# Kernel tuning notes

Hardware: AMD Instinct MI355X
Metric: run time of the kernel (lower is better)

The kernel has to match this reference:

```python
import jax, jax.numpy as jnp
import numpy as np

VOCAB, EMB, LAT, MAXLEN, BATCH = 2048, 256, 64, 32, 64
SIZE_LAT = 3.0  # size_lat_dim: initial upper bound of every latent dimension


def setup_inputs() -> dict:
    key = jax.random.key(0)
    k0, k1, k2, k3 = jax.random.split(key, 4)
    tokens = jax.random.randint(k0, (BATCH, MAXLEN), 1, VOCAB, dtype=jnp.int32)  # avoid PAD=0
    emb = jax.random.normal(k1, (VOCAB, EMB), jnp.float32) * 0.02
    Wx = jax.random.normal(k2, (EMB, 4 * VOCAB), jnp.float32) * (1.0 / np.sqrt(EMB))
    Wh = jax.random.normal(k3, (VOCAB, 4 * VOCAB), jnp.float32) * (1.0 / np.sqrt(VOCAB))
    b = jnp.zeros((4 * VOCAB,), jnp.float32)
    return {"tokens": tokens, "emb": emb, "Wx": Wx, "Wh": Wh, "b": b}


def _lstm_step(x, h, c, Wx, Wh, b):
    # Keras LSTM gate order: i, f, g(candidate), o
    z = x @ Wx + h @ Wh + b
    i, f, g, o = jnp.split(z, 4, axis=-1)
    c = jax.nn.sigmoid(f) * c + jax.nn.sigmoid(i) * jnp.tanh(g)
    h = jax.nn.sigmoid(o) * jnp.tanh(c)
    return h, c


def reference(tokens, emb, Wx, Wh, b):
    B = tokens.shape[0]
    low0 = jnp.zeros((B, LAT), jnp.float32)
    upp0 = jnp.full((B, LAT), SIZE_LAT, jnp.float32)
    h0 = jnp.zeros((B, VOCAB), jnp.float32)  # empty (all-PAD) prefix -> zero LSTM output -> uniform softmax
    c0 = jnp.zeros((B, VOCAB), jnp.float32)
    dims = jnp.arange(LAT)

    def step(carry, tok):
        low, upp, h, c, d = carry
        # LM distribution over next token given prefix consumed so far
        probs = jax.nn.softmax(h, axis=-1)                      # [B, V]
        cum = jnp.cumsum(probs, axis=-1)
        c_upp = jnp.take_along_axis(cum, tok[:, None], axis=-1)[:, 0]
        c_low = c_upp - jnp.take_along_axis(probs, tok[:, None], axis=-1)[:, 0]
        # arithmetic-coding bound update on current latent dimension d only
        mask = dims == d                                         # [LAT]
        rng = jnp.sum(jnp.where(mask, upp - low, 0.0), axis=-1)  # [B] range at dim d
        base = jnp.sum(jnp.where(mask, low, 0.0), axis=-1)       # [B] low at dim d
        low = jnp.where(mask[None, :], (base + rng * c_low)[:, None], low)
        upp = jnp.where(mask[None, :], (base + rng * c_upp)[:, None], upp)
        z = 0.5 * (low + upp)                                    # mean of stacked bounds
        # advance embedded LM by one token (equivalent to re-running it on the prefix)
        h, c = _lstm_step(emb[tok], h, c, Wx, Wh, b)
        d = (d + 1) % LAT
        return (low, upp, h, c, d), z

    _, zs = jax.lax.scan(step, (low0, upp0, h0, c0, jnp.int32(0)), tokens.T)
    return jnp.transpose(zs, (1, 0, 2))  # [B, MAXLEN, LAT]
```

## Files before the change

### kernel.cpp

```cpp
#include <hip/hip_runtime.h>
#include <hip/hip_bf16.h>

#define VOCAB 2048
#define EMBD  256
#define KTOT  2304
#define LATD  64
#define TLEN  32
#define BATCH 64
#define NBLK  256
#define NCG   128
#define AROW  2304
#define ASLOT (BATCH * AROW)

typedef __attribute__((ext_vector_type(4))) float f32x4;

__global__ void k_init(unsigned char* __restrict__ a8, unsigned* __restrict__ bar) {
  int i = blockIdx.x * 256 + threadIdx.x;
  if (i < 32768) {
    int row = i >> 9;
    *(unsigned*)(a8 + (size_t)row * AROW + ((i & 511) << 2)) = 0u;
  }
  if (i < 384) bar[i] = 0;
}

__global__ void k_conv(const float* __restrict__ src,
                       unsigned char* __restrict__ dst, int koff) {
  __shared__ unsigned char tile[64][80];
  int k0 = (blockIdx.x >> 7) * 64;
  int n0 = (blockIdx.x & 127) * 64;
  int tid = threadIdx.x;
  {
    int kl = tid >> 2;
    int nq = (tid & 3) << 4;
    const float* s = src + (size_t)(k0 + kl) * 8192 + n0 + nq;
#pragma unroll
    for (int i = 0; i < 4; ++i) {
      float4 v = *reinterpret_cast<const float4*>(s + i * 4);
      unsigned pa = (unsigned)__builtin_amdgcn_cvt_pk_fp8_f32(v.x * 32.f, v.y * 32.f, 0, false);
      unsigned pb = (unsigned)__builtin_amdgcn_cvt_pk_fp8_f32(v.z * 32.f, v.w * 32.f, 0, false);
      tile[nq + i * 4 + 0][kl] = (unsigned char)(pa & 0xFF);
      tile[nq + i * 4 + 1][kl] = (unsigned char)((pa >> 8) & 0xFF);
      tile[nq + i * 4 + 2][kl] = (unsigned char)(pb & 0xFF);
      tile[nq + i * 4 + 3][kl] = (unsigned char)((pb >> 8) & 0xFF);
    }
  }
  __syncthreads();
  {
    int nl = tid >> 2;
    int kq = (tid & 3) << 4;
    *(uint4*)(dst + (size_t)(n0 + nl) * AROW + koff + k0 + kq) =
        *(const uint4*)&tile[nl][kq];
  }
}

__global__ void k_gather(const int* __restrict__ tokens,
                         const float* __restrict__ emb,
                         unsigned char* __restrict__ a8) {
  int tid = threadIdx.x;
  int row = blockIdx.x * 4 + (tid >> 6);
  int lane = tid & 63;
  int t = row >> 6, b = row & 63;
  int tok = tokens[b * TLEN + t];
  float4 v = *reinterpret_cast<const float4*>(emb + (size_t)tok * EMBD + lane * 4);
  unsigned pa = (unsigned)__builtin_amdgcn_cvt_pk_fp8_f32(v.x * 256.f, v.y * 256.f, 0, false);
  unsigned pb = (unsigned)__builtin_amdgcn_cvt_pk_fp8_f32(v.z * 256.f, v.w * 256.f, 0, false);
  *(unsigned*)(a8 + (size_t)t * ASLOT + (size_t)b * AROW + 2048 + lane * 4) =
      (pa & 0xFFFFu) | (pb << 16);
}

__device__ __forceinline__ void store_agent_u32(unsigned* p, unsigned v) {
  __hip_atomic_store(p, v, __ATOMIC_RELAXED, __HIP_MEMORY_SCOPE_AGENT);
}
__device__ __forceinline__ unsigned load_agent_u32(const unsigned* p) {
  return __hip_atomic_load(p, __ATOMIC_RELAXED, __HIP_MEMORY_SCOPE_AGENT);
}
__device__ __forceinline__ unsigned long long load_agent_u64(const void* p) {
  return __hip_atomic_load((const unsigned long long*)p, __ATOMIC_RELAXED,
                           __HIP_MEMORY_SCOPE_AGENT);
}
__device__ __forceinline__ void store_agent_f32(float* p, float v) {
  __hip_atomic_store(p, v, __ATOMIC_RELAXED, __HIP_MEMORY_SCOPE_AGENT);
}
__device__ __forceinline__ float2 load_agent_f32x2(const float* p) {
  unsigned long long u = load_agent_u64(p);
  float2 f;
  __builtin_memcpy(&f, &u, 8);
  return f;
}

__device__ __forceinline__ void grid_barrier(unsigned* arrv, unsigned* rel,
                                             int t, int j, int tid, int lane) {
  __syncthreads();
  const unsigned want = (unsigned)(t + 1);
  if (j == 0) {
    if (tid < 64) {
      if (lane == 0) store_agent_u32(arrv, want);
      for (;;) {
        unsigned long long a = load_agent_u64(arrv + 2 * lane);
        unsigned long long b = load_agent_u64(arrv + 128 + 2 * lane);
        bool ok = ((unsigned)a >= want) && ((unsigned)(a >> 32) >= want) &&
                  ((unsigned)b >= want) && ((unsigned)(b >> 32) >= want);
        if (__all(ok)) break;
      }
      if (lane < 8) store_agent_u32(rel + (lane << 4), want);
    }
  } else {
    if (tid == 0) {
      store_agent_u32(arrv + j, want);
      while (load_agent_u32(rel + ((j & 7) << 4)) < want)
        __builtin_amdgcn_s_sleep(1);
    }
  }
  __syncthreads();
}

__global__ __launch_bounds__(512, 1) void k_persist(
    const int* __restrict__ tokens,
    const unsigned char* __restrict__ B8,
    unsigned char* __restrict__ a8,
    const float* __restrict__ bias,
    float* __restrict__ stats,
    float* __restrict__ out,
    unsigned* __restrict__ arrv,
    unsigned* __restrict__ rel) {
  const int tid = threadIdx.x;
  const int lane = tid & 63;
  const int wid = tid >> 6;
  const int j = blockIdx.x;
  const int cg = (j & 7) | ((j >> 4) << 3);
  const int rg = (j >> 3) & 1;
  const int r0 = rg << 5;

  __shared__ float racc[8][2][4][4][64];
  __shared__ float spart[TLEN][3];
  __shared__ float sval[TLEN];

  const int rr = lane & 15;
  const int kg = lane >> 4;

  long Bf[9][4];
  {
    const unsigned char* b8B[4];
#pragma unroll
    for (int gt = 0; gt < 4; ++gt)
      b8B[gt] = B8 + (size_t)((gt << 11) + (cg << 4) + rr) * AROW + wid * 288 + kg * 8;
#pragma unroll
    for (int it = 0; it < 9; ++it)
#pragma unroll
      for (int gt = 0; gt < 4; ++gt)
        Bf[it][gt] = *(const long*)(b8B[gt] + it * 32);
  }

  const int m_e = wid >> 2;
  const int r_e = wid & 3;
  const int rowg = r0 + m_e * 16 + kg * 4 + r_e;
  const int v = (cg << 4) + rr;
  float bias_r[4];
#pragma unroll
  for (int gt = 0; gt < 4; ++gt) bias_r[gt] = bias[gt * 2048 + v];
  float c_reg = 0.f;

  for (int t = 0; t < TLEN; ++t) {
    const int par = t & 1;
    const unsigned char* a8cur = a8 + (size_t)t * ASLOT;
    unsigned char* a8next = a8 + (size_t)(t + 1) * ASLOT;
    const int tnext = (t + 1 < TLEN) ? t + 1 : TLEN - 1;
    const int tok = tokens[rowg * TLEN + tnext];

    float2 sv;
    const bool do_stat = (t > 0) && (j < BATCH) && (wid < 3);
    if (do_stat)
      sv = load_agent_f32x2(stats + par * 3 * BATCH * NCG +
                            (wid * BATCH + j) * NCG + lane * 2);

    f32x4 acc[2][4];
#pragma unroll
    for (int mf = 0; mf < 2; ++mf)
#pragma unroll
      for (int gt = 0; gt < 4; ++gt) acc[mf][gt] = (f32x4){0.f, 0.f, 0.f, 0.f};

    const unsigned char* aB = a8cur + (size_t)(r0 + rr) * AROW + wid * 288 + kg * 8;
    long Ar[4][2];
    auto issue = [&](int it) {
      int slot = it & 3;
      Ar[slot][0] = *(const long*)(aB + it * 32);
      Ar[slot][1] = *(const long*)(aB + 16 * AROW + it * 32);
    };

#pragma unroll
    for (int it = 0; it < 4; ++it) issue(it);
#pragma unroll
    for (int it = 0; it < 9; ++it) {
      const int sl = it & 3;
#pragma unroll
      for (int gt = 0; gt < 4; ++gt) {
        acc[0][gt] = __builtin_amdgcn_mfma_f32_16x16x32_fp8_fp8(Ar[sl][0], Bf[it][gt], acc[0][gt], 0, 0, 0);
        acc[1][gt] = __builtin_amdgcn_mfma_f32_16x16x32_fp8_fp8(Ar[sl][1], Bf[it][gt], acc[1][gt], 0, 0, 0);
      }
      if (it + 4 < 9) issue(it + 4);
    }

#pragma unroll
    for (int mf = 0; mf < 2; ++mf)
#pragma unroll
      for (int gt = 0; gt < 4; ++gt)
#pragma unroll
        for (int r = 0; r < 4; ++r) racc[wid][mf][gt][r][lane] = acc[mf][gt][r];
    __syncthreads();

    if (do_stat) {
      float a = sv.x + sv.y;
#pragma unroll
      for (int mm = 1; mm <= 32; mm <<= 1) a += __shfl_xor(a, mm);
      if (lane == 0) spart[t][wid] = a;
    }

    float z[4];
#pragma unroll
    for (int gt = 0; gt < 4; ++gt) {
      float s = 0.f;
#pragma unroll
      for (int w = 0; w < 8; ++w) s += racc[w][m_e][gt][r_e][lane];
      z[gt] = s * (1.f / 8192.f) + bias_r[gt];
    }
    float gi = 1.f / (1.f + __expf(-z[0]));
    float gf = 1.f / (1.f + __expf(-z[1]));
    float go = 1.f / (1.f + __expf(-z[3]));
    float cnew = gf * c_reg + gi * tanhf(z[2]);
    float hn = go * tanhf(cnew);
    c_reg = cnew;

    {
      float hs = hn * 256.f;
      float hb = __shfl_xor(hs, 1);
      float lo = (rr & 1) ? hb : hs;
      float hi = (rr & 1) ? hs : hb;
      unsigned pk = (unsigned)__builtin_amdgcn_cvt_pk_fp8_f32(lo, hi, 0, false) & 0xFFFFu;
      unsigned pk2 = (unsigned)__shfl_xor((int)pk, 2);
      unsigned word = pk | (pk2 << 16);
      if ((rr & 3) == 0)
        store_agent_u32((unsigned*)(a8next + (size_t)rowg * AROW + v), word);
    }

    float e = __expf(hn);
    float sl = (v < tok) ? e : 0.f;
    float st = (v == tok) ? e : 0.f;
#pragma unroll
    for (int mm = 1; mm <= 8; mm <<= 1) {
      e += __shfl_xor(e, mm);
      sl += __shfl_xor(sl, mm);
      st += __shfl_xor(st, mm);
    }
    if (rr == 0) {
      float* stn = stats + (par ^ 1) * 3 * BATCH * NCG;
      store_agent_f32(&stn[(0 * BATCH + rowg) * NCG + cg], e);
      store_agent_f32(&stn[(1 * BATCH + rowg) * NCG + cg], sl);
      store_agent_f32(&stn[(2 * BATCH + rowg) * NCG + cg], st);
    }

    if (t < TLEN - 1) grid_barrier(arrv, rel, t, j, tid, lane);
  }

  if (j < BATCH) {
    __syncthreads();
    if (tid < TLEN) {
      float val;
      if (tid == 0) {
        int tk = tokens[j * TLEN];
        val = 1.5f * (2.f * tk + 1.f) * (1.f / 2048.f);
      } else {
        float S  = spart[tid][0];
        float SL = spart[tid][1];
        float ST = spart[tid][2];
        val = 1.5f * (2.f * SL + ST) / S;
      }
      sval[tid] = val;
    }
    __syncthreads();
    for (int idx = tid; idx < TLEN * LATD; idx += 512) {
      int tp = idx >> 6, d = idx & 63;
      out[j * TLEN * LATD + idx] = (d < TLEN && d <= tp) ? sval[d] : 1.5f;
    }
  }
}

extern "C" void kernel_launch(void* const* d_in, const int* in_sizes, int n_in,
                              void* d_out, int out_size, void* d_ws, size_t ws_size,
                              hipStream_t stream) {
  (void)in_sizes; (void)n_in; (void)out_size; (void)ws_size;
  const int* tokens = (const int*)d_in[0];
  const float* emb  = (const float*)d_in[1];
  const float* Wx   = (const float*)d_in[2];
  const float* Wh   = (const float*)d_in[3];
  const float* bias = (const float*)d_in[4];
  float* out = (float*)d_out;
  char* ws = (char*)d_ws;

  unsigned char* B8 = (unsigned char*)(ws);
  unsigned char* a8 = (unsigned char*)(ws + 18874368);
  float* stats      = (float*)(ws + 23740416);
  unsigned* arrv    = (unsigned*)(ws + 23937024);
  unsigned* rel     = (unsigned*)(ws + 23938048);

  k_init<<<512, 256, 0, stream>>>(a8, arrv);
  k_conv<<<4096, 256, 0, stream>>>(Wh, B8, 0);
  k_conv<<<512, 256, 0, stream>>>(Wx, B8, 2048);
  k_gather<<<512, 256, 0, stream>>>(tokens, emb, a8);
  k_persist<<<NBLK, 512, 0, stream>>>(tokens, B8, a8, bias, stats, out, arrv, rel);
}
```

Before: 258.6 us.

## Split batch into two independent chains with decentralized arrival-counter waits

Each block now owns 8 vocab columns across all 64 batch rows, instead of 16 columns for one half of the batch. The batch is processed as two 32-row chains, each with its own arrival array. The centralized master/release grid barrier is replaced by every block polling all 256 arrival counters, which lets one chain's compute overlap the other chain's synchronization latency. The last LSTM step, whose hidden state is never consumed, is skipped and the final stats are gathered after a last wait. Trade-offs are more polling traffic from all blocks, smaller MFMA tiles per chain, and fully loading A operands before issuing MFMAs.

```diff
diff --git a/kernel.cpp b/kernel.cpp
--- a/kernel.cpp
+++ b/kernel.cpp
@@ -2,25 +2,22 @@
 #include <hip/hip_bf16.h>
 
 #define VOCAB 2048
-#define EMBD  256
-#define KTOT  2304
-#define LATD  64
+#define AROW  2304
 #define TLEN  32
 #define BATCH 64
 #define NBLK  256
-#define NCG   128
-#define AROW  2304
+#define NCG   256
 #define ASLOT (BATCH * AROW)
 
 typedef __attribute__((ext_vector_type(4))) float f32x4;
 
-__global__ void k_init(unsigned char* __restrict__ a8, unsigned* __restrict__ bar) {
+__global__ void k_init(unsigned char* __restrict__ a8, unsigned* __restrict__ arrv) {
   int i = blockIdx.x * 256 + threadIdx.x;
   if (i < 32768) {
     int row = i >> 9;
     *(unsigned*)(a8 + (size_t)row * AROW + ((i & 511) << 2)) = 0u;
   }
-  if (i < 384) bar[i] = 0;
+  if (i < 512) arrv[i] = 0;
 }
 
 __global__ void k_conv(const float* __restrict__ src,
@@ -61,7 +58,7 @@
   int lane = tid & 63;
   int t = row >> 6, b = row & 63;
   int tok = tokens[b * TLEN + t];
-  float4 v = *reinterpret_cast<const float4*>(emb + (size_t)tok * EMBD + lane * 4);
+  float4 v = *reinterpret_cast<const float4*>(emb + (size_t)tok * 256 + lane * 4);
   unsigned pa = (unsigned)__builtin_amdgcn_cvt_pk_fp8_f32(v.x * 256.f, v.y * 256.f, 0, false);
   unsigned pb = (unsigned)__builtin_amdgcn_cvt_pk_fp8_f32(v.z * 256.f, v.w * 256.f, 0, false);
   *(unsigned*)(a8 + (size_t)t * ASLOT + (size_t)b * AROW + 2048 + lane * 4) =
@@ -70,9 +67,6 @@
 
 __device__ __forceinline__ void store_agent_u32(unsigned* p, unsigned v) {
   __hip_atomic_store(p, v, __ATOMIC_RELAXED, __HIP_MEMORY_SCOPE_AGENT);
-}
-__device__ __forceinline__ unsigned load_agent_u32(const unsigned* p) {
-  return __hip_atomic_load(p, __ATOMIC_RELAXED, __HIP_MEMORY_SCOPE_AGENT);
 }
 __device__ __forceinline__ unsigned long long load_agent_u64(const void* p) {
   return __hip_atomic_load((const unsigned long long*)p, __ATOMIC_RELAXED,
@@ -88,27 +82,16 @@
   return f;
 }
 
-__device__ __forceinline__ void grid_barrier(unsigned* arrv, unsigned* rel,
-                                             int t, int j, int tid, int lane) {
-  __syncthreads();
-  const unsigned want = (unsigned)(t + 1);
-  if (j == 0) {
-    if (tid < 64) {
-      if (lane == 0) store_agent_u32(arrv, want);
-      for (;;) {
-        unsigned long long a = load_agent_u64(arrv + 2 * lane);
-        unsigned long long b = load_agent_u64(arrv + 128 + 2 * lane);
-        bool ok = ((unsigned)a >= want) && ((unsigned)(a >> 32) >= want) &&
-                  ((unsigned)b >= want) && ((unsigned)(b >> 32) >= want);
-        if (__all(ok)) break;
-      }
-      if (lane < 8) store_agent_u32(rel + (lane << 4), want);
-    }
-  } else {
-    if (tid == 0) {
-      store_agent_u32(arrv + j, want);
-      while (load_agent_u32(rel + ((j & 7) << 4)) < want)
-        __builtin_amdgcn_s_sleep(1);
+__device__ __forceinline__ void chain_wait(unsigned* arrv, unsigned want,
+                                           int tid, int lane) {
+  if (tid < 64) {
+    for (;;) {
+      unsigned long long a = load_agent_u64(arrv + 2 * lane);
+      unsigned long long b = load_agent_u64(arrv + 128 + 2 * lane);
+      bool ok = ((unsigned)a >= want) && ((unsigned)(a >> 32) >= want) &&
+                ((unsigned)b >= want) && ((unsigned)(b >> 32) >= want);
+      if (__all(ok)) break;
+      __builtin_amdgcn_s_sleep(2);
     }
   }
   __syncthreads();
@@ -121,147 +104,167 @@
     const float* __restrict__ bias,
     float* __restrict__ stats,
     float* __restrict__ out,
-    unsigned* __restrict__ arrv,
-    unsigned* __restrict__ rel) {
+    unsigned* __restrict__ arrvA,
+    unsigned* __restrict__ arrvB) {
   const int tid = threadIdx.x;
   const int lane = tid & 63;
   const int wid = tid >> 6;
   const int j = blockIdx.x;
-  const int cg = (j & 7) | ((j >> 4) << 3);
-  const int rg = (j >> 3) & 1;
-  const int r0 = rg << 5;
-
-  __shared__ float racc[8][2][4][4][64];
+  const int cg = j;
+
+  __shared__ float racc[8][2][2][4][64];
   __shared__ float spart[TLEN][3];
   __shared__ float sval[TLEN];
 
   const int rr = lane & 15;
   const int kg = lane >> 4;
-
-  long Bf[9][4];
-  {
-    const unsigned char* b8B[4];
-#pragma unroll
-    for (int gt = 0; gt < 4; ++gt)
-      b8B[gt] = B8 + (size_t)((gt << 11) + (cg << 4) + rr) * AROW + wid * 288 + kg * 8;
-#pragma unroll
-    for (int it = 0; it < 9; ++it)
-#pragma unroll
-      for (int gt = 0; gt < 4; ++gt)
-        Bf[it][gt] = *(const long*)(b8B[gt] + it * 32);
-  }
-
-  const int m_e = wid >> 2;
-  const int r_e = wid & 3;
-  const int rowg = r0 + m_e * 16 + kg * 4 + r_e;
-  const int v = (cg << 4) + rr;
-  float bias_r[4];
-#pragma unroll
-  for (int gt = 0; gt < 4; ++gt) bias_r[gt] = bias[gt * 2048 + v];
-  float c_reg = 0.f;
-
-  for (int t = 0; t < TLEN; ++t) {
+  const int s_ = rr >> 3;
+  const int v = (cg << 3) + (rr & 7);
+
+  long Bf[9][2];
+#pragma unroll
+  for (int nf = 0; nf < 2; ++nf) {
+    const unsigned char* bp = B8 + (size_t)(((nf * 2 + s_) << 11) + v) * AROW +
+                              wid * 288 + kg * 8;
+#pragma unroll
+    for (int it = 0; it < 9; ++it) Bf[it][nf] = *(const long*)(bp + it * 32);
+  }
+
+  const float bias0 = bias[s_ * 2048 + v];
+  const float bias1 = bias[(2 + s_) * 2048 + v];
+  const int m_e = wid >> 2, r_e = wid & 3;
+  float c_reg[2] = {0.f, 0.f};
+
+  for (int t = 0; t <= 30; ++t) {
     const int par = t & 1;
     const unsigned char* a8cur = a8 + (size_t)t * ASLOT;
-    unsigned char* a8next = a8 + (size_t)(t + 1) * ASLOT;
-    const int tnext = (t + 1 < TLEN) ? t + 1 : TLEN - 1;
-    const int tok = tokens[rowg * TLEN + tnext];
-
-    float2 sv;
-    const bool do_stat = (t > 0) && (j < BATCH) && (wid < 3);
-    if (do_stat)
-      sv = load_agent_f32x2(stats + par * 3 * BATCH * NCG +
-                            (wid * BATCH + j) * NCG + lane * 2);
-
-    f32x4 acc[2][4];
-#pragma unroll
-    for (int mf = 0; mf < 2; ++mf)
-#pragma unroll
-      for (int gt = 0; gt < 4; ++gt) acc[mf][gt] = (f32x4){0.f, 0.f, 0.f, 0.f};
-
-    const unsigned char* aB = a8cur + (size_t)(r0 + rr) * AROW + wid * 288 + kg * 8;
-    long Ar[4][2];
-    auto issue = [&](int it) {
-      int slot = it & 3;
-      Ar[slot][0] = *(const long*)(aB + it * 32);
-      Ar[slot][1] = *(const long*)(aB + 16 * AROW + it * 32);
-    };
-
-#pragma unroll
-    for (int it = 0; it < 4; ++it) issue(it);
-#pragma unroll
-    for (int it = 0; it < 9; ++it) {
-      const int sl = it & 3;
-#pragma unroll
-      for (int gt = 0; gt < 4; ++gt) {
-        acc[0][gt] = __builtin_amdgcn_mfma_f32_16x16x32_fp8_fp8(Ar[sl][0], Bf[it][gt], acc[0][gt], 0, 0, 0);
-        acc[1][gt] = __builtin_amdgcn_mfma_f32_16x16x32_fp8_fp8(Ar[sl][1], Bf[it][gt], acc[1][gt], 0, 0, 0);
-      }
-      if (it + 4 < 9) issue(it + 4);
-    }
-
-#pragma unroll
-    for (int mf = 0; mf < 2; ++mf)
-#pragma unroll
-      for (int gt = 0; gt < 4; ++gt)
-#pragma unroll
-        for (int r = 0; r < 4; ++r) racc[wid][mf][gt][r][lane] = acc[mf][gt][r];
-    __syncthreads();
-
-    if (do_stat) {
-      float a = sv.x + sv.y;
+    unsigned char* a8nxt = a8 + (size_t)(t + 1) * ASLOT;
+
+#pragma unroll
+    for (int ch = 0; ch < 2; ++ch) {
+      const int r0 = ch << 5;
+      unsigned* arrv = ch ? arrvB : arrvA;
+
+      if (t > 0) chain_wait(arrv, (unsigned)t, tid, lane);
+
+      float2 sva, svb;
+      const bool do_stat = (t > 0) && (j >= r0) && (j < r0 + 32) && (wid < 3);
+      if (do_stat) {
+        const float* st = stats + par * 3 * BATCH * NCG +
+                          (wid * BATCH + j) * NCG + lane * 4;
+        sva = load_agent_f32x2(st);
+        svb = load_agent_f32x2(st + 2);
+      }
+
+      f32x4 acc[2][2];
+#pragma unroll
+      for (int mf = 0; mf < 2; ++mf)
+#pragma unroll
+        for (int nf = 0; nf < 2; ++nf) acc[mf][nf] = (f32x4){0.f, 0.f, 0.f, 0.f};
+
+      long Aw[9][2];
+      {
+        const unsigned char* ap = a8cur + (size_t)(r0 + rr) * AROW + wid * 288 + kg * 8;
+#pragma unroll
+        for (int it = 0; it < 9; ++it) {
+          Aw[it][0] = *(const long*)(ap + it * 32);
+          Aw[it][1] = *(const long*)(ap + 16 * AROW + it * 32);
+        }
+      }
+#pragma unroll
+      for (int it = 0; it < 9; ++it)
+#pragma unroll
+        for (int mf = 0; mf < 2; ++mf)
+#pragma unroll
+          for (int nf = 0; nf < 2; ++nf)
+            acc[mf][nf] = __builtin_amdgcn_mfma_f32_16x16x32_fp8_fp8(
+                Aw[it][mf], Bf[it][nf], acc[mf][nf], 0, 0, 0);
+
+#pragma unroll
+      for (int mf = 0; mf < 2; ++mf)
+#pragma unroll
+        for (int nf = 0; nf < 2; ++nf)
+#pragma unroll
+          for (int r = 0; r < 4; ++r) racc[wid][mf][nf][r][lane] = acc[mf][nf][r];
+      __syncthreads();
+
+      if (do_stat) {
+        float a = sva.x + sva.y + svb.x + svb.y;
+#pragma unroll
+        for (int mm = 1; mm <= 32; mm <<= 1) a += __shfl_xor(a, mm);
+        if (lane == 0) spart[t][wid] = a;
+      }
+
+      const int rowg = r0 + m_e * 16 + kg * 4 + r_e;
+      float z0 = 0.f, z1 = 0.f;
+#pragma unroll
+      for (int w = 0; w < 8; ++w) {
+        z0 += racc[w][m_e][0][r_e][lane];
+        z1 += racc[w][m_e][1][r_e][lane];
+      }
+      z0 = z0 * (1.f / 8192.f) + bias0;
+      z1 = z1 * (1.f / 8192.f) + bias1;
+      float o0 = __shfl_xor(z0, 8);
+      float o1 = __shfl_xor(z1, 8);
+      float zi = s_ ? o0 : z0;
+      float zf = s_ ? z0 : o0;
+      float zg = s_ ? o1 : z1;
+      float zo = s_ ? z1 : o1;
+      float gi = 1.f / (1.f + __expf(-zi));
+      float gf = 1.f / (1.f + __expf(-zf));
+      float go = 1.f / (1.f + __expf(-zo));
+      float cnew = gf * c_reg[ch] + gi * tanhf(zg);
+      float hn = go * tanhf(cnew);
+      c_reg[ch] = cnew;
+
+      if (t < 30) {
+        float hs = hn * 256.f;
+        float hb = __shfl_xor(hs, 1);
+        float lo = (rr & 1) ? hb : hs;
+        float hi = (rr & 1) ? hs : hb;
+        unsigned pk = (unsigned)__builtin_amdgcn_cvt_pk_fp8_f32(lo, hi, 0, false) & 0xFFFFu;
+        unsigned pk2 = (unsigned)__shfl_xor((int)pk, 2);
+        unsigned word = pk | (pk2 << 16);
+        if (!s_ && (rr & 3) == 0)
+          store_agent_u32((unsigned*)(a8nxt + (size_t)rowg * AROW + v), word);
+      }
+
+      {
+        int tok = tokens[rowg * TLEN + t + 1];
+        float e = __expf(hn);
+        float sl = (v < tok) ? e : 0.f;
+        float st_ = (v == tok) ? e : 0.f;
+#pragma unroll
+        for (int mm = 1; mm <= 4; mm <<= 1) {
+          e += __shfl_xor(e, mm);
+          sl += __shfl_xor(sl, mm);
+          st_ += __shfl_xor(st_, mm);
+        }
+        if (rr == 0) {
+          float* stn = stats + (par ^ 1) * 3 * BATCH * NCG;
+          store_agent_f32(&stn[(0 * BATCH + rowg) * NCG + cg], e);
+          store_agent_f32(&stn[(1 * BATCH + rowg) * NCG + cg], sl);
+          store_agent_f32(&stn[(2 * BATCH + rowg) * NCG + cg], st_);
+        }
+      }
+
+      __syncthreads();
+      if (tid == 0) store_agent_u32(arrv + j, (unsigned)(t + 1));
+    }
+  }
+
+  if (j < BATCH) {
+    chain_wait((j < 32) ? arrvA : arrvB, 31u, tid, lane);
+    if (wid < 3) {
+      const float* st = stats + 1 * 3 * BATCH * NCG +
+                        (wid * BATCH + j) * NCG + lane * 4;
+      float2 a_ = load_agent_f32x2(st);
+      float2 b_ = load_agent_f32x2(st + 2);
+      float a = a_.x + a_.y + b_.x + b_.y;
 #pragma unroll
       for (int mm = 1; mm <= 32; mm <<= 1) a += __shfl_xor(a, mm);
-      if (lane == 0) spart[t][wid] = a;
-    }
-
-    float z[4];
-#pragma unroll
-    for (int gt = 0; gt < 4; ++gt) {
-      float s = 0.f;
-#pragma unroll
-      for (int w = 0; w < 8; ++w) s += racc[w][m_e][gt][r_e][lane];
-      z[gt] = s * (1.f / 8192.f) + bias_r[gt];
-    }
-    float gi = 1.f / (1.f + __expf(-z[0]));
-    float gf = 1.f / (1.f + __expf(-z[1]));
-    float go = 1.f / (1.f + __expf(-z[3]));
-    float cnew = gf * c_reg + gi * tanhf(z[2]);
-    float hn = go * tanhf(cnew);
-    c_reg = cnew;
-
-    {
-      float hs = hn * 256.f;
-      float hb = __shfl_xor(hs, 1);
-      float lo = (rr & 1) ? hb : hs;
-      float hi = (rr & 1) ? hs : hb;
-      unsigned pk = (unsigned)__builtin_amdgcn_cvt_pk_fp8_f32(lo, hi, 0, false) & 0xFFFFu;
-      unsigned pk2 = (unsigned)__shfl_xor((int)pk, 2);
-      unsigned word = pk | (pk2 << 16);
-      if ((rr & 3) == 0)
-        store_agent_u32((unsigned*)(a8next + (size_t)rowg * AROW + v), word);
-    }
-
-    float e = __expf(hn);
-    float sl = (v < tok) ? e : 0.f;
-    float st = (v == tok) ? e : 0.f;
-#pragma unroll
-    for (int mm = 1; mm <= 8; mm <<= 1) {
-      e += __shfl_xor(e, mm);
-      sl += __shfl_xor(sl, mm);
-      st += __shfl_xor(st, mm);
-    }
-    if (rr == 0) {
-      float* stn = stats + (par ^ 1) * 3 * BATCH * NCG;
-      store_agent_f32(&stn[(0 * BATCH + rowg) * NCG + cg], e);
-      store_agent_f32(&stn[(1 * BATCH + rowg) * NCG + cg], sl);
-      store_agent_f32(&stn[(2 * BATCH + rowg) * NCG + cg], st);
-    }
-
-    if (t < TLEN - 1) grid_barrier(arrv, rel, t, j, tid, lane);
-  }
-
-  if (j < BATCH) {
+      if (lane == 0) spart[31][wid] = a;
+    }
     __syncthreads();
     if (tid < TLEN) {
       float val;
@@ -277,9 +280,9 @@
       sval[tid] = val;
     }
     __syncthreads();
-    for (int idx = tid; idx < TLEN * LATD; idx += 512) {
+    for (int idx = tid; idx < TLEN * 64; idx += 512) {
       int tp = idx >> 6, d = idx & 63;
-      out[j * TLEN * LATD + idx] = (d < TLEN && d <= tp) ? sval[d] : 1.5f;
+      out[j * TLEN * 64 + idx] = (d < TLEN && d <= tp) ? sval[d] : 1.5f;
     }
   }
 }
@@ -299,12 +302,12 @@
   unsigned char* B8 = (unsigned char*)(ws);
   unsigned char* a8 = (unsigned char*)(ws + 18874368);
   float* stats      = (float*)(ws + 23740416);
-  unsigned* arrv    = (unsigned*)(ws + 23937024);
-  unsigned* rel     = (unsigned*)(ws + 23938048);
-
-  k_init<<<512, 256, 0, stream>>>(a8, arrv);
+  unsigned* arrvA   = (unsigned*)(ws + 24133632);
+  unsigned* arrvB   = (unsigned*)(ws + 24134656);
+
+  k_init<<<512, 256, 0, stream>>>(a8, arrvA);
   k_conv<<<4096, 256, 0, stream>>>(Wh, B8, 0);
   k_conv<<<512, 256, 0, stream>>>(Wx, B8, 2048);
   k_gather<<<512, 256, 0, stream>>>(tokens, emb, a8);
-  k_persist<<<NBLK, 512, 0, stream>>>(tokens, B8, a8, bias, stats, out, arrv, rel);
-}
+  k_persist<<<NBLK, 512, 0, stream>>>(tokens, B8, a8, bias, stats, out, arrvA, arrvB);
+}
```

New measurement: 413.0 us. +59.7%, slower.

## Split grid barrier into per-row-group half barriers and drop final LSTM step

Applied to the files above, without the earlier changes.

Replaces the single 256-block grid barrier with two independent barriers, one per 32-row batch half (128 blocks each), since each row group only reads its own rows of the activation buffer. The loop now runs 31 steps instead of 32, skipping the final LSTM step whose hidden state is never consumed. The last softmax statistics are read after the final barrier, and output writes are remapped to the owning block of each batch row. This cuts barrier fan-in and removes one full matmul step, at the cost of more complex indexing and correctness that depends on the half-partitioning of data dependencies.

```diff
diff --git a/kernel.cpp b/kernel.cpp
--- a/kernel.cpp
+++ b/kernel.cpp
@@ -3,7 +3,6 @@
 
 #define VOCAB 2048
 #define EMBD  256
-#define KTOT  2304
 #define LATD  64
 #define TLEN  32
 #define BATCH 64
@@ -11,6 +10,7 @@
 #define NCG   128
 #define AROW  2304
 #define ASLOT (BATCH * AROW)
+#define BARW  512
 
 typedef __attribute__((ext_vector_type(4))) float f32x4;
 
@@ -20,7 +20,7 @@
     int row = i >> 9;
     *(unsigned*)(a8 + (size_t)row * AROW + ((i & 511) << 2)) = 0u;
   }
-  if (i < 384) bar[i] = 0;
+  if (i < BARW) bar[i] = 0;
 }
 
 __global__ void k_conv(const float* __restrict__ src,
@@ -88,26 +88,26 @@
   return f;
 }
 
-__device__ __forceinline__ void grid_barrier(unsigned* arrv, unsigned* rel,
-                                             int t, int j, int tid, int lane) {
+__device__ __forceinline__ void half_barrier(unsigned* bar, int t, int cg,
+                                             int rg, int xg, int tid, int lane) {
   __syncthreads();
   const unsigned want = (unsigned)(t + 1);
-  if (j == 0) {
+  unsigned* hArr = bar + rg * 128;
+  unsigned* hRel = bar + 256;
+  if (cg == 0) {
     if (tid < 64) {
-      if (lane == 0) store_agent_u32(arrv, want);
+      if (lane == 0) store_agent_u32(hArr, want);
       for (;;) {
-        unsigned long long a = load_agent_u64(arrv + 2 * lane);
-        unsigned long long b = load_agent_u64(arrv + 128 + 2 * lane);
-        bool ok = ((unsigned)a >= want) && ((unsigned)(a >> 32) >= want) &&
-                  ((unsigned)b >= want) && ((unsigned)(b >> 32) >= want);
+        unsigned long long a = load_agent_u64(hArr + 2 * lane);
+        bool ok = ((unsigned)a >= want) && ((unsigned)(a >> 32) >= want);
         if (__all(ok)) break;
       }
-      if (lane < 8) store_agent_u32(rel + (lane << 4), want);
+      if (lane < 8) store_agent_u32(hRel + ((rg * 8 + lane) << 4), want);
     }
   } else {
     if (tid == 0) {
-      store_agent_u32(arrv + j, want);
-      while (load_agent_u32(rel + ((j & 7) << 4)) < want)
+      store_agent_u32(hArr + cg, want);
+      while (load_agent_u32(hRel + ((rg * 8 + xg) << 4)) < want)
         __builtin_amdgcn_s_sleep(1);
     }
   }
@@ -121,15 +121,16 @@
     const float* __restrict__ bias,
     float* __restrict__ stats,
     float* __restrict__ out,
-    unsigned* __restrict__ arrv,
-    unsigned* __restrict__ rel) {
+    unsigned* __restrict__ bar) {
   const int tid = threadIdx.x;
   const int lane = tid & 63;
   const int wid = tid >> 6;
   const int j = blockIdx.x;
   const int cg = (j & 7) | ((j >> 4) << 3);
   const int rg = (j >> 3) & 1;
+  const int xg = j & 7;
   const int r0 = rg << 5;
+  const int b_own = r0 + cg;
 
   __shared__ float racc[8][2][4][4][64];
   __shared__ float spart[TLEN][3];
@@ -160,18 +161,17 @@
   for (int gt = 0; gt < 4; ++gt) bias_r[gt] = bias[gt * 2048 + v];
   float c_reg = 0.f;
 
-  for (int t = 0; t < TLEN; ++t) {
+  for (int t = 0; t <= 30; ++t) {
     const int par = t & 1;
     const unsigned char* a8cur = a8 + (size_t)t * ASLOT;
     unsigned char* a8next = a8 + (size_t)(t + 1) * ASLOT;
-    const int tnext = (t + 1 < TLEN) ? t + 1 : TLEN - 1;
-    const int tok = tokens[rowg * TLEN + tnext];
+    const int tok = tokens[rowg * TLEN + t + 1];
 
     float2 sv;
-    const bool do_stat = (t > 0) && (j < BATCH) && (wid < 3);
+    const bool do_stat = (t > 0) && (cg < 32) && (wid < 3);
     if (do_stat)
       sv = load_agent_f32x2(stats + par * 3 * BATCH * NCG +
-                            (wid * BATCH + j) * NCG + lane * 2);
+                            (wid * BATCH + b_own) * NCG + lane * 2);
 
     f32x4 acc[2][4];
 #pragma unroll
@@ -230,7 +230,7 @@
     float hn = go * tanhf(cnew);
     c_reg = cnew;
 
-    {
+    if (t < 30) {
       float hs = hn * 256.f;
       float hb = __shfl_xor(hs, 1);
       float lo = (rr & 1) ? hb : hs;
@@ -258,15 +258,23 @@
       store_agent_f32(&stn[(2 * BATCH + rowg) * NCG + cg], st);
     }
 
-    if (t < TLEN - 1) grid_barrier(arrv, rel, t, j, tid, lane);
-  }
-
-  if (j < BATCH) {
+    half_barrier(bar, t, cg, rg, xg, tid, lane);
+  }
+
+  if (cg < 32) {
+    if (wid < 3) {
+      float2 sv = load_agent_f32x2(stats + 1 * 3 * BATCH * NCG +
+                                   (wid * BATCH + b_own) * NCG + lane * 2);
+      float a = sv.x + sv.y;
+#pragma unroll
+      for (int mm = 1; mm <= 32; mm <<= 1) a += __shfl_xor(a, mm);
+      if (lane == 0) spart[31][wid] = a;
+    }
     __syncthreads();
     if (tid < TLEN) {
       float val;
       if (tid == 0) {
-        int tk = tokens[j * TLEN];
+        int tk = tokens[b_own * TLEN];
         val = 1.5f * (2.f * tk + 1.f) * (1.f / 2048.f);
       } else {
         float S  = spart[tid][0];
@@ -279,7 +287,7 @@
     __syncthreads();
     for (int idx = tid; idx < TLEN * LATD; idx += 512) {
       int tp = idx >> 6, d = idx & 63;
-      out[j * TLEN * LATD + idx] = (d < TLEN && d <= tp) ? sval[d] : 1.5f;
+      out[b_own * TLEN * LATD + idx] = (d < TLEN && d <= tp) ? sval[d] : 1.5f;
     }
   }
 }
@@ -299,12 +307,11 @@
   unsigned char* B8 = (unsigned char*)(ws);
   unsigned char* a8 = (unsigned char*)(ws + 18874368);
   float* stats      = (float*)(ws + 23740416);
-  unsigned* arrv    = (unsigned*)(ws + 23937024);
-  unsigned* rel     = (unsigned*)(ws + 23938048);
-
-  k_init<<<512, 256, 0, stream>>>(a8, arrv);
+  unsigned* bar     = (unsigned*)(ws + 23937024);
+
+  k_init<<<512, 256, 0, stream>>>(a8, bar);
   k_conv<<<4096, 256, 0, stream>>>(Wh, B8, 0);
   k_conv<<<512, 256, 0, stream>>>(Wx, B8, 2048);
   k_gather<<<512, 256, 0, stream>>>(tokens, emb, a8);
-  k_persist<<<NBLK, 512, 0, stream>>>(tokens, B8, a8, bias, stats, out, arrv, rel);
-}
+  k_persist<<<NBLK, 512, 0, stream>>>(tokens, B8, a8, bias, stats, out, bar);
+}
```

Result: faster. 247.3 us (-4.4%).

## Merge prep kernels into one launch and drop the final LSTM timestep

Applied to the files above, without the earlier changes.

Combines the init, weight conversion and embedding-gather kernels into a single k_prep launch, which cuts launch overhead and inter-kernel gaps. The persistent kernel now runs 31 timesteps instead of 32, because the last LSTM step's output is never used, and it skips writing h on the last iteration. The final stats are read after the loop. Stats-owning blocks are remapped so they spread across row groups, which changes which blocks finish up the output.

```diff
diff --git a/kernel.cpp b/kernel.cpp
--- a/kernel.cpp
+++ b/kernel.cpp
@@ -3,7 +3,6 @@
 
 #define VOCAB 2048
 #define EMBD  256
-#define KTOT  2304
 #define LATD  64
 #define TLEN  32
 #define BATCH 64
@@ -14,60 +13,6 @@
 
 typedef __attribute__((ext_vector_type(4))) float f32x4;
 
-__global__ void k_init(unsigned char* __restrict__ a8, unsigned* __restrict__ bar) {
-  int i = blockIdx.x * 256 + threadIdx.x;
-  if (i < 32768) {
-    int row = i >> 9;
-    *(unsigned*)(a8 + (size_t)row * AROW + ((i & 511) << 2)) = 0u;
-  }
-  if (i < 384) bar[i] = 0;
-}
-
-__global__ void k_conv(const float* __restrict__ src,
-                       unsigned char* __restrict__ dst, int koff) {
-  __shared__ unsigned char tile[64][80];
-  int k0 = (blockIdx.x >> 7) * 64;
-  int n0 = (blockIdx.x & 127) * 64;
-  int tid = threadIdx.x;
-  {
-    int kl = tid >> 2;
-    int nq = (tid & 3) << 4;
-    const float* s = src + (size_t)(k0 + kl) * 8192 + n0 + nq;
-#pragma unroll
-    for (int i = 0; i < 4; ++i) {
-      float4 v = *reinterpret_cast<const float4*>(s + i * 4);
-      unsigned pa = (unsigned)__builtin_amdgcn_cvt_pk_fp8_f32(v.x * 32.f, v.y * 32.f, 0, false);
-      unsigned pb = (unsigned)__builtin_amdgcn_cvt_pk_fp8_f32(v.z * 32.f, v.w * 32.f, 0, false);
-      tile[nq + i * 4 + 0][kl] = (unsigned char)(pa & 0xFF);
-      tile[nq + i * 4 + 1][kl] = (unsigned char)((pa >> 8) & 0xFF);
-      tile[nq + i * 4 + 2][kl] = (unsigned char)(pb & 0xFF);
-      tile[nq + i * 4 + 3][kl] = (unsigned char)((pb >> 8) & 0xFF);
-    }
-  }
-  __syncthreads();
-  {
-    int nl = tid >> 2;
-    int kq = (tid & 3) << 4;
-    *(uint4*)(dst + (size_t)(n0 + nl) * AROW + koff + k0 + kq) =
-        *(const uint4*)&tile[nl][kq];
-  }
-}
-
-__global__ void k_gather(const int* __restrict__ tokens,
-                         const float* __restrict__ emb,
-                         unsigned char* __restrict__ a8) {
-  int tid = threadIdx.x;
-  int row = blockIdx.x * 4 + (tid >> 6);
-  int lane = tid & 63;
-  int t = row >> 6, b = row & 63;
-  int tok = tokens[b * TLEN + t];
-  float4 v = *reinterpret_cast<const float4*>(emb + (size_t)tok * EMBD + lane * 4);
-  unsigned pa = (unsigned)__builtin_amdgcn_cvt_pk_fp8_f32(v.x * 256.f, v.y * 256.f, 0, false);
-  unsigned pb = (unsigned)__builtin_amdgcn_cvt_pk_fp8_f32(v.z * 256.f, v.w * 256.f, 0, false);
-  *(unsigned*)(a8 + (size_t)t * ASLOT + (size_t)b * AROW + 2048 + lane * 4) =
-      (pa & 0xFFFFu) | (pb << 16);
-}
-
 __device__ __forceinline__ void store_agent_u32(unsigned* p, unsigned v) {
   __hip_atomic_store(p, v, __ATOMIC_RELAXED, __HIP_MEMORY_SCOPE_AGENT);
 }
@@ -86,6 +31,66 @@
   float2 f;
   __builtin_memcpy(&f, &u, 8);
   return f;
+}
+
+__global__ void k_prep(const int* __restrict__ tokens,
+                       const float* __restrict__ emb,
+                       const float* __restrict__ Wh,
+                       const float* __restrict__ Wx,
+                       unsigned char* __restrict__ B8,
+                       unsigned char* __restrict__ a8,
+                       unsigned* __restrict__ bar) {
+  __shared__ unsigned char tile[64][80];
+  const int bid = blockIdx.x;
+  const int tid = threadIdx.x;
+
+  if (bid < 4608) {
+    const float* src = (bid < 4096) ? Wh : Wx;
+    const int koff = (bid < 4096) ? 0 : 2048;
+    const int lb = (bid < 4096) ? bid : bid - 4096;
+    int k0 = (lb >> 7) * 64;
+    int n0 = (lb & 127) * 64;
+    {
+      int kl = tid >> 2;
+      int nq = (tid & 3) << 4;
+      const float* s = src + (size_t)(k0 + kl) * 8192 + n0 + nq;
+#pragma unroll
+      for (int i = 0; i < 4; ++i) {
+        float4 v = *reinterpret_cast<const float4*>(s + i * 4);
+        unsigned pa = (unsigned)__builtin_amdgcn_cvt_pk_fp8_f32(v.x * 32.f, v.y * 32.f, 0, false);
+        unsigned pb = (unsigned)__builtin_amdgcn_cvt_pk_fp8_f32(v.z * 32.f, v.w * 32.f, 0, false);
+        tile[nq + i * 4 + 0][kl] = (unsigned char)(pa & 0xFF);
+        tile[nq + i * 4 + 1][kl] = (unsigned char)((pa >> 8) & 0xFF);
+        tile[nq + i * 4 + 2][kl] = (unsigned char)(pb & 0xFF);
+        tile[nq + i * 4 + 3][kl] = (unsigned char)((pb >> 8) & 0xFF);
+      }
+    }
+    __syncthreads();
+    {
+      int nl = tid >> 2;
+      int kq = (tid & 3) << 4;
+      *(uint4*)(B8 + (size_t)(n0 + nl) * AROW + koff + k0 + kq) =
+          *(const uint4*)&tile[nl][kq];
+    }
+  } else if (bid < 5120) {
+    int lb = bid - 4608;
+    int row = lb * 4 + (tid >> 6);
+    int lane = tid & 63;
+    int t = row >> 6, b = row & 63;
+    int tok = tokens[b * TLEN + t];
+    float4 v = *reinterpret_cast<const float4*>(emb + (size_t)tok * EMBD + lane * 4);
+    unsigned pa = (unsigned)__builtin_amdgcn_cvt_pk_fp8_f32(v.x * 256.f, v.y * 256.f, 0, false);
+    unsigned pb = (unsigned)__builtin_amdgcn_cvt_pk_fp8_f32(v.z * 256.f, v.w * 256.f, 0, false);
+    *(unsigned*)(a8 + (size_t)t * ASLOT + (size_t)b * AROW + 2048 + lane * 4) =
+        (pa & 0xFFFFu) | (pb << 16);
+  } else {
+    int i = (bid - 5120) * 256 + tid;
+    if (i < 32768) {
+      int row = i >> 9;
+      *(unsigned*)(a8 + (size_t)row * AROW + ((i & 511) << 2)) = 0u;
+    }
+    if (i < 384) bar[i] = 0;
+  }
 }
 
 __device__ __forceinline__ void grid_barrier(unsigned* arrv, unsigned* rel,
@@ -130,6 +135,7 @@
   const int cg = (j & 7) | ((j >> 4) << 3);
   const int rg = (j >> 3) & 1;
   const int r0 = rg << 5;
+  const int b_own = r0 + cg;
 
   __shared__ float racc[8][2][4][4][64];
   __shared__ float spart[TLEN][3];
@@ -160,18 +166,17 @@
   for (int gt = 0; gt < 4; ++gt) bias_r[gt] = bias[gt * 2048 + v];
   float c_reg = 0.f;
 
-  for (int t = 0; t < TLEN; ++t) {
+  for (int t = 0; t <= 30; ++t) {
     const int par = t & 1;
     const unsigned char* a8cur = a8 + (size_t)t * ASLOT;
     unsigned char* a8next = a8 + (size_t)(t + 1) * ASLOT;
-    const int tnext = (t + 1 < TLEN) ? t + 1 : TLEN - 1;
-    const int tok = tokens[rowg * TLEN + tnext];
+    const int tok = tokens[rowg * TLEN + t + 1];
 
     float2 sv;
-    const bool do_stat = (t > 0) && (j < BATCH) && (wid < 3);
+    const bool do_stat = (t > 0) && (cg < 32) && (wid < 3);
     if (do_stat)
       sv = load_agent_f32x2(stats + par * 3 * BATCH * NCG +
-                            (wid * BATCH + j) * NCG + lane * 2);
+                            (wid * BATCH + b_own) * NCG + lane * 2);
 
     f32x4 acc[2][4];
 #pragma unroll
@@ -230,7 +235,7 @@
     float hn = go * tanhf(cnew);
     c_reg = cnew;
 
-    {
+    if (t < 30) {
       float hs = hn * 256.f;
       float hb = __shfl_xor(hs, 1);
       float lo = (rr & 1) ? hb : hs;
@@ -258,15 +263,23 @@
       store_agent_f32(&stn[(2 * BATCH + rowg) * NCG + cg], st);
     }
 
-    if (t < TLEN - 1) grid_barrier(arrv, rel, t, j, tid, lane);
-  }
-
-  if (j < BATCH) {
+    grid_barrier(arrv, rel, t, j, tid, lane);
+  }
+
+  if (cg < 32) {
+    if (wid < 3) {
+      float2 sv = load_agent_f32x2(stats + 1 * 3 * BATCH * NCG +
+                                   (wid * BATCH + b_own) * NCG + lane * 2);
+      float a = sv.x + sv.y;
+#pragma unroll
+      for (int mm = 1; mm <= 32; mm <<= 1) a += __shfl_xor(a, mm);
+      if (lane == 0) spart[31][wid] = a;
+    }
     __syncthreads();
     if (tid < TLEN) {
       float val;
       if (tid == 0) {
-        int tk = tokens[j * TLEN];
+        int tk = tokens[b_own * TLEN];
         val = 1.5f * (2.f * tk + 1.f) * (1.f / 2048.f);
       } else {
         float S  = spart[tid][0];
@@ -279,7 +292,7 @@
     __syncthreads();
     for (int idx = tid; idx < TLEN * LATD; idx += 512) {
       int tp = idx >> 6, d = idx & 63;
-      out[j * TLEN * LATD + idx] = (d < TLEN && d <= tp) ? sval[d] : 1.5f;
+      out[b_own * TLEN * LATD + idx] = (d < TLEN && d <= tp) ? sval[d] : 1.5f;
     }
   }
 }
@@ -302,9 +315,6 @@
   unsigned* arrv    = (unsigned*)(ws + 23937024);
   unsigned* rel     = (unsigned*)(ws + 23938048);
 
-  k_init<<<512, 256, 0, stream>>>(a8, arrv);
-  k_conv<<<4096, 256, 0, stream>>>(Wh, B8, 0);
-  k_conv<<<512, 256, 0, stream>>>(Wx, B8, 2048);
-  k_gather<<<512, 256, 0, stream>>>(tokens, emb, a8);
+  k_prep<<<5632, 256, 0, stream>>>(tokens, emb, Wh, Wx, B8, a8, arrv);
   k_persist<<<NBLK, 512, 0, stream>>>(tokens, B8, a8, bias, stats, out, arrv, rel);
 }
```

New measurement: 250.4 us. 1.03x faster.
